# Optimization experiments

Hardware: AMD Instinct MI355X
Metric: run time of the kernel (lower is better)

The kernel has to match this reference:

```python
import jax, jax.numpy as jnp
import numpy as np


def setup_inputs() -> dict:
    key = jax.random.key(0)
    B, T, M, K = 256, 1024, 63, 128
    IN = M + 1
    ks = jax.random.split(key, 12)
    bound_lstm = 1.0 / np.sqrt(K)        # k = 1/out_features
    bound_v = 1.0 / np.sqrt(K)           # nn.Linear(k, m) default init bound
    def u(k, shape, b):
        return jax.random.uniform(k, shape, jnp.float32, -b, b)
    inputs = jax.random.normal(ks[0], (B, T, IN), jnp.float32)
    return {
        "inputs": inputs,
        "Wi": u(ks[1], (K, IN), bound_lstm), "Ui": u(ks[2], (K, K), bound_lstm),
        "Wf": u(ks[3], (K, IN), bound_lstm), "Uf": u(ks[4], (K, K), bound_lstm),
        "Wg": u(ks[5], (K, IN), bound_lstm), "Ug": u(ks[6], (K, K), bound_lstm),
        "Wo": u(ks[7], (K, IN), bound_lstm), "Uo": u(ks[8], (K, K), bound_lstm),
        "Vw": u(ks[9], (M, K), bound_v),     "Vb": u(ks[10], (M,), bound_v),
    }


def reference(inputs, Wi, Ui, Wf, Uf, Wg, Ug, Wo, Uo, Vw, Vb):
    B, T, IN = inputs.shape
    K = Wi.shape[0]
    # Fuse the 4 gate projections into one GEMM per step (same math).
    Wx = jnp.concatenate([Wi, Wf, Wg, Wo], axis=0)  # [4K, IN]
    Uh = jnp.concatenate([Ui, Uf, Ug, Uo], axis=0)  # [4K, K]

    xs = jnp.swapaxes(inputs, 0, 1)  # [T, B, IN]

    def step(carry, x_t):
        h_prev, c_prev = carry
        z = x_t @ Wx.T + h_prev @ Uh.T          # [B, 4K]
        zi, zf, zg, zo = jnp.split(z, 4, axis=-1)
        i = jax.nn.sigmoid(zi)
        f = jax.nn.sigmoid(zf)
        g = jnp.tanh(zg)
        o = jax.nn.sigmoid(zo)
        c = f * c_prev + i * g
        h = o * jnp.tanh(c_prev)                # NOTE: source uses c_prev, not c
        y = h @ Vw.T + Vb                       # [B, M]
        return (h, c), y

    h0 = jnp.zeros((B, K), inputs.dtype)
    c0 = jnp.zeros((B, K), inputs.dtype)
    _, ys = jax.lax.scan(step, (h0, c0), xs)    # ys: [T, B, M]
    return jnp.swapaxes(ys, 0, 1)               # [B, T, M]
```

## Files before the change

### kernel.cpp

```cpp
#include <hip/hip_runtime.h>
#include <math.h>

typedef _Float16 h2 __attribute__((ext_vector_type(2)));
typedef unsigned int u32;

#define T_STEPS 1024
#define B_SZ    256
#define K_DIM   128
#define IN_DIM  64
#define M_DIM   63
#define NTH     512
#define ZP_STRIDE 516

__device__ __forceinline__ h2 as_h2(u32 v) { union { u32 u; h2 h; } c; c.u = v; return c.h; }

#if __has_builtin(__builtin_amdgcn_fdot2)
__device__ __forceinline__ float dot2(h2 a, h2 b, float acc) {
    return __builtin_amdgcn_fdot2(a, b, acc, false);
}
#else
__device__ __forceinline__ float dot2(h2 a, h2 b, float acc) {
    return acc + (float)a.x * (float)b.x + (float)a.y * (float)b.y;
}
#endif

__device__ __forceinline__ float fast_sigmoid(float z) {
    return __builtin_amdgcn_rcpf(1.0f + __expf(-z));
}
__device__ __forceinline__ float fast_tanh(float z) {
    z = fminf(15.0f, fmaxf(-15.0f, z));
    float t = __expf(2.0f * z);
    return (t - 1.0f) * __builtin_amdgcn_rcpf(t + 1.0f);
}

__device__ __forceinline__ void block_sync_lds() {
    asm volatile("s_waitcnt lgkmcnt(0)\n\ts_barrier" ::: "memory");
}

__global__ __launch_bounds__(NTH)
void lstm_fused(const float* __restrict__ x,
                const float* __restrict__ Wi, const float* __restrict__ Ui,
                const float* __restrict__ Wf, const float* __restrict__ Uf,
                const float* __restrict__ Wg, const float* __restrict__ Ug,
                const float* __restrict__ Wo, const float* __restrict__ Uo,
                const float* __restrict__ Vw, const float* __restrict__ Vb,
                float* __restrict__ out)
{
    __shared__ __align__(16) h2    hx[2][96];
    __shared__ __align__(16) float zpart[4][ZP_STRIDE];

    const int b   = blockIdx.x;
    const int tid = threadIdx.x;

    const int rg   = tid >> 2;
    const int cb   = tid & 3;
    const int row0 = rg * 4;
    const int gate = row0 >> 7;
    const int rr   = row0 & 127;
    const float* Ub = (gate == 0) ? Ui : (gate == 1) ? Uf : (gate == 2) ? Ug : Uo;
    const float* Wb = (gate == 0) ? Wi : (gate == 1) ? Wf : (gate == 2) ? Wg : Wo;

    h2 w[4][24];
    #pragma unroll
    for (int j = 0; j < 4; ++j) {
        #pragma unroll
        for (int i = 0; i < 24; ++i) {
            int c0 = 2 * (cb * 24 + i);
            const float* s = (c0 < K_DIM) ? (Ub + (rr + j) * K_DIM + c0)
                                          : (Wb + (rr + j) * IN_DIM + (c0 - K_DIM));
            float2 v = *(const float2*)s;
            w[j][i] = h2{(_Float16)v.x, (_Float16)v.y};
        }
    }

    const int r2 = tid - 256;
    const int ym = r2 >> 2;
    const int yj = r2 & 3;
    const bool is_y = (tid >= 256 && tid < 508);
    h2 vwreg[16];
    float vbv = 0.0f;
    if (is_y) {
        const float* src = Vw + ym * K_DIM + yj * 32;
        #pragma unroll
        for (int i = 0; i < 16; ++i)
            vwreg[i] = h2{(_Float16)src[2 * i], (_Float16)src[2 * i + 1]};
        if (yj == 0) vbv = Vb[ym];
    }

    const size_t xbase = (size_t)b * T_STEPS * IN_DIM;
    const size_t obase = (size_t)b * T_STEPS * M_DIM;

    if (tid < 64) hx[0][tid] = h2{(_Float16)0.f, (_Float16)0.f};
    if (tid >= 128 && tid < 192)
        ((_Float16*)hx[0])[128 + (tid - 128)] = (_Float16)x[xbase + (tid - 128)];
    float c = 0.0f;

    __syncthreads();

    for (int t = 0; t < T_STEPS; ++t) {
        const int par = t & 1;

        float xv = 0.0f;
        if (t + 1 < T_STEPS && tid >= 128 && tid < 192)
            xv = x[xbase + (size_t)(t + 1) * IN_DIM + (tid - 128)];

        float p0 = 0.f, p1 = 0.f, p2 = 0.f, p3 = 0.f;
        const uint4* A = (const uint4*)(&hx[par][cb * 24]);
        #pragma unroll
        for (int q = 0; q < 6; ++q) {
            uint4 av = A[q];
            h2 a0 = as_h2(av.x), a1 = as_h2(av.y), a2 = as_h2(av.z), a3 = as_h2(av.w);
            p0 = dot2(w[0][q*4+0], a0, p0); p0 = dot2(w[0][q*4+1], a1, p0);
            p0 = dot2(w[0][q*4+2], a2, p0); p0 = dot2(w[0][q*4+3], a3, p0);
            p1 = dot2(w[1][q*4+0], a0, p1); p1 = dot2(w[1][q*4+1], a1, p1);
            p1 = dot2(w[1][q*4+2], a2, p1); p1 = dot2(w[1][q*4+3], a3, p1);
            p2 = dot2(w[2][q*4+0], a0, p2); p2 = dot2(w[2][q*4+1], a1, p2);
            p2 = dot2(w[2][q*4+2], a2, p2); p2 = dot2(w[2][q*4+3], a3, p2);
            p3 = dot2(w[3][q*4+0], a0, p3); p3 = dot2(w[3][q*4+1], a1, p3);
            p3 = dot2(w[3][q*4+2], a2, p3); p3 = dot2(w[3][q*4+3], a3, p3);
        }
        *(float4*)&zpart[cb][row0] = make_float4(p0, p1, p2, p3);

        block_sync_lds();

        if (tid < 128) {
            float zi = zpart[0][tid]       + zpart[1][tid]
                     + zpart[2][tid]       + zpart[3][tid];
            float zf = zpart[0][128 + tid] + zpart[1][128 + tid]
                     + zpart[2][128 + tid] + zpart[3][128 + tid];
            float zg = zpart[0][256 + tid] + zpart[1][256 + tid]
                     + zpart[2][256 + tid] + zpart[3][256 + tid];
            float zo = zpart[0][384 + tid] + zpart[1][384 + tid]
                     + zpart[2][384 + tid] + zpart[3][384 + tid];
            float gi = fast_sigmoid(zi);
            float gf = fast_sigmoid(zf);
            float gg = fast_tanh(zg);
            float go = fast_sigmoid(zo);
            float tc = fast_tanh(c);
            float hn = go * tc;
            c = gf * c + gi * gg;
            ((_Float16*)hx[par ^ 1])[tid] = (_Float16)hn;
        } else if (tid < 192) {
            if (t + 1 < T_STEPS)
                ((_Float16*)hx[par ^ 1])[128 + (tid - 128)] = (_Float16)xv;
        } else if (is_y && t > 0) {
            const uint4* hv = (const uint4*)(&hx[par][yj * 16]);
            float p = 0.f;
            #pragma unroll
            for (int q = 0; q < 4; ++q) {
                uint4 h4v = hv[q];
                p = dot2(vwreg[q*4+0], as_h2(h4v.x), p);
                p = dot2(vwreg[q*4+1], as_h2(h4v.y), p);
                p = dot2(vwreg[q*4+2], as_h2(h4v.z), p);
                p = dot2(vwreg[q*4+3], as_h2(h4v.w), p);
            }
            p += __shfl_xor(p, 1);
            p += __shfl_xor(p, 2);
            if (yj == 0) out[obase + (size_t)(t - 1) * M_DIM + ym] = p + vbv;
        }

        block_sync_lds();
    }

    if (is_y) {
        const uint4* hv = (const uint4*)(&hx[0][yj * 16]);
        float p = 0.f;
        #pragma unroll
        for (int q = 0; q < 4; ++q) {
            uint4 h4v = hv[q];
            p = dot2(vwreg[q*4+0], as_h2(h4v.x), p);
            p = dot2(vwreg[q*4+1], as_h2(h4v.y), p);
            p = dot2(vwreg[q*4+2], as_h2(h4v.z), p);
            p = dot2(vwreg[q*4+3], as_h2(h4v.w), p);
        }
        p += __shfl_xor(p, 1);
        p += __shfl_xor(p, 2);
        if (yj == 0) out[obase + (size_t)(T_STEPS - 1) * M_DIM + ym] = p + vbv;
    }
}

extern "C" void kernel_launch(void* const* d_in, const int* in_sizes, int n_in,
                              void* d_out, int out_size, void* d_ws, size_t ws_size,
                              hipStream_t stream) {
    const float* x  = (const float*)d_in[0];
    const float* Wi = (const float*)d_in[1];
    const float* Ui = (const float*)d_in[2];
    const float* Wf = (const float*)d_in[3];
    const float* Uf = (const float*)d_in[4];
    const float* Wg = (const float*)d_in[5];
    const float* Ug = (const float*)d_in[6];
    const float* Wo = (const float*)d_in[7];
    const float* Uo = (const float*)d_in[8];
    const float* Vw = (const float*)d_in[9];
    const float* Vb = (const float*)d_in[10];
    float* out = (float*)d_out;

    lstm_fused<<<dim3(B_SZ), dim3(NTH), 0, stream>>>(
        x, Wi, Ui, Wf, Uf, Wg, Ug, Wo, Uo, Vw, Vb, out);
}
```

Measured before the change: 878.8 us.

## Replace LDS partial-sum reduction with shuffle transpose-reduce, one barrier per step

The gate partial sums no longer go through a shared zpart buffer. Each group of 8 lanes now handles two hidden units times four gates, and a butterfly shuffle transpose-reduce gives each lane one gate pre-activation. The gate activations are then exchanged across lanes by shuffles, which removes one of the two block barriers per timestep. The output projection is computed by every thread alongside the gate GEMV instead of in a separate role, which adds ALU work and shuffles to each step in exchange for shorter critical-path latency.

```diff
diff --git a/kernel.cpp b/kernel.cpp
--- a/kernel.cpp
+++ b/kernel.cpp
@@ -10,7 +10,6 @@
 #define IN_DIM  64
 #define M_DIM   63
 #define NTH     512
-#define ZP_STRIDE 516
 
 __device__ __forceinline__ h2 as_h2(u32 v) { union { u32 u; h2 h; } c; c.u = v; return c.h; }
 
@@ -23,15 +22,6 @@
     return acc + (float)a.x * (float)b.x + (float)a.y * (float)b.y;
 }
 #endif
-
-__device__ __forceinline__ float fast_sigmoid(float z) {
-    return __builtin_amdgcn_rcpf(1.0f + __expf(-z));
-}
-__device__ __forceinline__ float fast_tanh(float z) {
-    z = fminf(15.0f, fmaxf(-15.0f, z));
-    float t = __expf(2.0f * z);
-    return (t - 1.0f) * __builtin_amdgcn_rcpf(t + 1.0f);
-}
 
 __device__ __forceinline__ void block_sync_lds() {
     asm volatile("s_waitcnt lgkmcnt(0)\n\ts_barrier" ::: "memory");
@@ -46,136 +36,147 @@
                 const float* __restrict__ Vw, const float* __restrict__ Vb,
                 float* __restrict__ out)
 {
-    __shared__ __align__(16) h2    hx[2][96];
-    __shared__ __align__(16) float zpart[4][ZP_STRIDE];
+    __shared__ __align__(16) h2 hx[2][96];
 
     const int b   = blockIdx.x;
     const int tid = threadIdx.x;
-
-    const int rg   = tid >> 2;
-    const int cb   = tid & 3;
-    const int row0 = rg * 4;
-    const int gate = row0 >> 7;
-    const int rr   = row0 & 127;
-    const float* Ub = (gate == 0) ? Ui : (gate == 1) ? Uf : (gate == 2) ? Ug : Uo;
-    const float* Wb = (gate == 0) ? Wi : (gate == 1) ? Wf : (gate == 2) ? Wg : Wo;
-
-    h2 w[4][24];
+    const int rg  = tid >> 3;
+    const int cb  = tid & 7;
+    const int lane_g = tid & 3;
+    const int kown   = tid >> 2;
+
+    h2 w[8][12];
     #pragma unroll
-    for (int j = 0; j < 4; ++j) {
-        #pragma unroll
-        for (int i = 0; i < 24; ++i) {
-            int c0 = 2 * (cb * 24 + i);
-            const float* s = (c0 < K_DIM) ? (Ub + (rr + j) * K_DIM + c0)
-                                          : (Wb + (rr + j) * IN_DIM + (c0 - K_DIM));
+    for (int c = 0; c < 8; ++c) {
+        const int gate = c & 3;
+        const int k    = 2 * rg + (c >> 2);
+        const float* U = (gate == 0) ? Ui : (gate == 1) ? Uf : (gate == 2) ? Ug : Uo;
+        const float* W = (gate == 0) ? Wi : (gate == 1) ? Wf : (gate == 2) ? Wg : Wo;
+        const float* urow = U + k * K_DIM;
+        const float* wrow = W + k * IN_DIM;
+        #pragma unroll
+        for (int i = 0; i < 12; ++i) {
+            int j = cb * 12 + i;
+            const float* s = (j < 64) ? (urow + 2 * j) : (wrow + 2 * (j - 64));
             float2 v = *(const float2*)s;
-            w[j][i] = h2{(_Float16)v.x, (_Float16)v.y};
-        }
-    }
-
-    const int r2 = tid - 256;
-    const int ym = r2 >> 2;
-    const int yj = r2 & 3;
-    const bool is_y = (tid >= 256 && tid < 508);
-    h2 vwreg[16];
+            w[c][i] = h2{(_Float16)v.x, (_Float16)v.y};
+        }
+    }
+
+    const int  ym   = rg;
+    const bool is_y = (tid < 504);
+    h2 vwreg[8] = {};
     float vbv = 0.0f;
     if (is_y) {
-        const float* src = Vw + ym * K_DIM + yj * 32;
-        #pragma unroll
-        for (int i = 0; i < 16; ++i)
+        const float* src = Vw + ym * K_DIM + cb * 16;
+        #pragma unroll
+        for (int i = 0; i < 8; ++i)
             vwreg[i] = h2{(_Float16)src[2 * i], (_Float16)src[2 * i + 1]};
-        if (yj == 0) vbv = Vb[ym];
+        if (cb == 0) vbv = Vb[ym];
     }
 
     const size_t xbase = (size_t)b * T_STEPS * IN_DIM;
     const size_t obase = (size_t)b * T_STEPS * M_DIM;
 
-    if (tid < 64) hx[0][tid] = h2{(_Float16)0.f, (_Float16)0.f};
-    if (tid >= 128 && tid < 192)
-        ((_Float16*)hx[0])[128 + (tid - 128)] = (_Float16)x[xbase + (tid - 128)];
+    if (tid < 64) {
+        hx[0][tid] = h2{(_Float16)0.f, (_Float16)0.f};
+        ((_Float16*)hx[0])[128 + tid] = (_Float16)x[xbase + tid];
+    }
     float c = 0.0f;
-
     __syncthreads();
 
     for (int t = 0; t < T_STEPS; ++t) {
         const int par = t & 1;
 
         float xv = 0.0f;
-        if (t + 1 < T_STEPS && tid >= 128 && tid < 192)
-            xv = x[xbase + (size_t)(t + 1) * IN_DIM + (tid - 128)];
-
-        float p0 = 0.f, p1 = 0.f, p2 = 0.f, p3 = 0.f;
-        const uint4* A = (const uint4*)(&hx[par][cb * 24]);
-        #pragma unroll
-        for (int q = 0; q < 6; ++q) {
-            uint4 av = A[q];
+        if (t + 1 < T_STEPS && tid < 64)
+            xv = x[xbase + (size_t)(t + 1) * IN_DIM + tid];
+
+        float tc;
+        {
+            float e = __expf(-2.0f * c);
+            tc = 2.0f * __builtin_amdgcn_rcpf(1.0f + e) - 1.0f;
+        }
+
+        float p0 = 0.f, p1 = 0.f, p2 = 0.f, p3 = 0.f,
+              p4 = 0.f, p5 = 0.f, p6 = 0.f, p7 = 0.f;
+        const uint4* A = (const uint4*)hx[par];
+        #pragma unroll
+        for (int q = 0; q < 3; ++q) {
+            uint4 av = A[cb * 3 + q];
             h2 a0 = as_h2(av.x), a1 = as_h2(av.y), a2 = as_h2(av.z), a3 = as_h2(av.w);
-            p0 = dot2(w[0][q*4+0], a0, p0); p0 = dot2(w[0][q*4+1], a1, p0);
-            p0 = dot2(w[0][q*4+2], a2, p0); p0 = dot2(w[0][q*4+3], a3, p0);
-            p1 = dot2(w[1][q*4+0], a0, p1); p1 = dot2(w[1][q*4+1], a1, p1);
-            p1 = dot2(w[1][q*4+2], a2, p1); p1 = dot2(w[1][q*4+3], a3, p1);
-            p2 = dot2(w[2][q*4+0], a0, p2); p2 = dot2(w[2][q*4+1], a1, p2);
-            p2 = dot2(w[2][q*4+2], a2, p2); p2 = dot2(w[2][q*4+3], a3, p2);
-            p3 = dot2(w[3][q*4+0], a0, p3); p3 = dot2(w[3][q*4+1], a1, p3);
-            p3 = dot2(w[3][q*4+2], a2, p3); p3 = dot2(w[3][q*4+3], a3, p3);
-        }
-        *(float4*)&zpart[cb][row0] = make_float4(p0, p1, p2, p3);
+#define GDOT(c_, pc) pc = dot2(w[c_][q*4+0], a0, pc); pc = dot2(w[c_][q*4+1], a1, pc); \
+                     pc = dot2(w[c_][q*4+2], a2, pc); pc = dot2(w[c_][q*4+3], a3, pc);
+            GDOT(0, p0) GDOT(1, p1) GDOT(2, p2) GDOT(3, p3)
+            GDOT(4, p4) GDOT(5, p5) GDOT(6, p6) GDOT(7, p7)
+#undef GDOT
+        }
+
+        float py = 0.f;
+        #pragma unroll
+        for (int q = 0; q < 2; ++q) {
+            uint4 hv = A[cb * 2 + q];
+            py = dot2(vwreg[q*4+0], as_h2(hv.x), py);
+            py = dot2(vwreg[q*4+1], as_h2(hv.y), py);
+            py = dot2(vwreg[q*4+2], as_h2(hv.z), py);
+            py = dot2(vwreg[q*4+3], as_h2(hv.w), py);
+        }
+
+        const bool b0 = (cb & 1), b1 = (cb >> 1) & 1, b2 = (cb >> 2) & 1;
+        float s0, s1, s2, s3, u0, u1, z;
+        { float ka, sa;
+          ka = b0 ? p1 : p0; sa = b0 ? p0 : p1; s0 = ka + __shfl_xor(sa, 1);
+          ka = b0 ? p3 : p2; sa = b0 ? p2 : p3; s1 = ka + __shfl_xor(sa, 1);
+          ka = b0 ? p5 : p4; sa = b0 ? p4 : p5; s2 = ka + __shfl_xor(sa, 1);
+          ka = b0 ? p7 : p6; sa = b0 ? p6 : p7; s3 = ka + __shfl_xor(sa, 1);
+          ka = b1 ? s1 : s0; sa = b1 ? s0 : s1; u0 = ka + __shfl_xor(sa, 2);
+          ka = b1 ? s3 : s2; sa = b1 ? s2 : s3; u1 = ka + __shfl_xor(sa, 2);
+          ka = b2 ? u1 : u0; sa = b2 ? u0 : u1; z  = ka + __shfl_xor(sa, 4);
+        }
+
+        const bool isg = (lane_g == 2);
+        float sc = isg ? 2.0f : 1.0f;
+        float e  = __expf(-sc * z);
+        float sg = __builtin_amdgcn_rcpf(1.0f + e);
+        float a  = isg ? 2.0f * sg - 1.0f : sg;
+
+        float af = __shfl_xor(a, 1);
+        float ag = __shfl_xor(a, 2);
+        float ao = __shfl_xor(af, 2);
+
+        float hn = ao * tc;
+        c = af * c + a * ag;
+
+        if (lane_g == 0)
+            ((_Float16*)hx[par ^ 1])[kown] = (_Float16)hn;
+        if (t + 1 < T_STEPS && tid < 64)
+            ((_Float16*)hx[par ^ 1])[128 + tid] = (_Float16)xv;
+
+        py += __shfl_xor(py, 1);
+        py += __shfl_xor(py, 2);
+        py += __shfl_xor(py, 4);
+        if (t > 0 && is_y && cb == 0)
+            out[obase + (size_t)(t - 1) * M_DIM + ym] = py + vbv;
 
         block_sync_lds();
-
-        if (tid < 128) {
-            float zi = zpart[0][tid]       + zpart[1][tid]
-                     + zpart[2][tid]       + zpart[3][tid];
-            float zf = zpart[0][128 + tid] + zpart[1][128 + tid]
-                     + zpart[2][128 + tid] + zpart[3][128 + tid];
-            float zg = zpart[0][256 + tid] + zpart[1][256 + tid]
-                     + zpart[2][256 + tid] + zpart[3][256 + tid];
-            float zo = zpart[0][384 + tid] + zpart[1][384 + tid]
-                     + zpart[2][384 + tid] + zpart[3][384 + tid];
-            float gi = fast_sigmoid(zi);
-            float gf = fast_sigmoid(zf);
-            float gg = fast_tanh(zg);
-            float go = fast_sigmoid(zo);
-            float tc = fast_tanh(c);
-            float hn = go * tc;
-            c = gf * c + gi * gg;
-            ((_Float16*)hx[par ^ 1])[tid] = (_Float16)hn;
-        } else if (tid < 192) {
-            if (t + 1 < T_STEPS)
-                ((_Float16*)hx[par ^ 1])[128 + (tid - 128)] = (_Float16)xv;
-        } else if (is_y && t > 0) {
-            const uint4* hv = (const uint4*)(&hx[par][yj * 16]);
-            float p = 0.f;
-            #pragma unroll
-            for (int q = 0; q < 4; ++q) {
-                uint4 h4v = hv[q];
-                p = dot2(vwreg[q*4+0], as_h2(h4v.x), p);
-                p = dot2(vwreg[q*4+1], as_h2(h4v.y), p);
-                p = dot2(vwreg[q*4+2], as_h2(h4v.z), p);
-                p = dot2(vwreg[q*4+3], as_h2(h4v.w), p);
-            }
-            p += __shfl_xor(p, 1);
-            p += __shfl_xor(p, 2);
-            if (yj == 0) out[obase + (size_t)(t - 1) * M_DIM + ym] = p + vbv;
-        }
-
-        block_sync_lds();
-    }
-
-    if (is_y) {
-        const uint4* hv = (const uint4*)(&hx[0][yj * 16]);
-        float p = 0.f;
-        #pragma unroll
-        for (int q = 0; q < 4; ++q) {
-            uint4 h4v = hv[q];
-            p = dot2(vwreg[q*4+0], as_h2(h4v.x), p);
-            p = dot2(vwreg[q*4+1], as_h2(h4v.y), p);
-            p = dot2(vwreg[q*4+2], as_h2(h4v.z), p);
-            p = dot2(vwreg[q*4+3], as_h2(h4v.w), p);
-        }
-        p += __shfl_xor(p, 1);
-        p += __shfl_xor(p, 2);
-        if (yj == 0) out[obase + (size_t)(T_STEPS - 1) * M_DIM + ym] = p + vbv;
+    }
+
+    {
+        const uint4* H = (const uint4*)hx[0];
+        float py = 0.f;
+        #pragma unroll
+        for (int q = 0; q < 2; ++q) {
+            uint4 hv = H[cb * 2 + q];
+            py = dot2(vwreg[q*4+0], as_h2(hv.x), py);
+            py = dot2(vwreg[q*4+1], as_h2(hv.y), py);
+            py = dot2(vwreg[q*4+2], as_h2(hv.z), py);
+            py = dot2(vwreg[q*4+3], as_h2(hv.w), py);
+        }
+        py += __shfl_xor(py, 1);
+        py += __shfl_xor(py, 2);
+        py += __shfl_xor(py, 4);
+        if (is_y && cb == 0)
+            out[obase + (size_t)(T_STEPS - 1) * M_DIM + ym] = py + vbv;
     }
 }
 
```

New measurement: 949.9 us. 8.1% more time.
